# Kernel optimization log

Measured on AMD Instinct MI355X. Metric: run time of the kernel, lower is better.

The kernel has to match this reference:

```python
import jax, jax.numpy as jnp
import numpy as np

D, HEADS, PTS, NQ, BEV_H, BEV_W, NCLS, BS, NL = 256, 8, 4, 900, 200, 200, 10, 4, 6
HD = D // HEADS
PC = (-51.2, -51.2, -5.0, 51.2, 51.2, 3.0)


def _ln(x, w, b):
    m = x.mean(-1, keepdims=True)
    v = ((x - m) ** 2).mean(-1, keepdims=True)
    return (x - m) * jax.lax.rsqrt(v + 1e-5) * w + b


def _inv_sig(x, eps=1e-5):
    x = jnp.clip(x, 0.0, 1.0)
    return jnp.log(jnp.clip(x, eps, None) / jnp.clip(1.0 - x, eps, None))


def _mha(q_in, k_in, v_in, in_w, in_b, out_w, out_b):
    # torch nn.MultiheadAttention (eval, dropout=0): packed in_proj (3D,D)
    b, n, _ = q_in.shape
    qw, kw, vw = jnp.split(in_w, 3, axis=0)
    qb, kb, vb = jnp.split(in_b, 3, axis=0)
    q = (q_in @ qw.T + qb).reshape(b, n, HEADS, HD)
    k = (k_in @ kw.T + kb).reshape(b, k_in.shape[1], HEADS, HD)
    v = (v_in @ vw.T + vb).reshape(b, v_in.shape[1], HEADS, HD)
    s = jnp.einsum('bqhd,bkhd->bhqk', q, k) * (1.0 / float(np.sqrt(HD)))
    a = jax.nn.softmax(s, axis=-1)
    o = jnp.einsum('bhqk,bkhd->bqhd', a, v).reshape(b, n, D)
    return o @ out_w.T + out_b


def _deform_attn(q, identity, value, ref2d, off_w, off_b, aw_w, aw_b, vp_w, vp_b, op_w, op_b):
    # CustomMSDeformableAttention, num_levels=1, num_points=4; bilinear grid_sample
    # semantics: align_corners=False, zero padding.
    b, n, _ = q.shape
    hw = value.shape[1]
    v = (value @ vp_w.T + vp_b).reshape(b, hw, HEADS, HD)
    vg = v.transpose(0, 2, 1, 3)  # (b, heads, HW, hd)
    off = (q @ off_w.T + off_b).reshape(b, n, HEADS, PTS, 2)
    aw = jax.nn.softmax((q @ aw_w.T + aw_b).reshape(b, n, HEADS, PTS), axis=-1)
    norm = jnp.array([BEV_W, BEV_H], jnp.float32)  # offset_normalizer = (W, H)
    loc = ref2d[:, :, None, None, :] + off / norm  # (b,n,heads,P,2) in [0,1]
    # grid_sample align_corners=False pixel coords
    x = (loc[..., 0] * BEV_W - 0.5).transpose(0, 2, 1, 3)  # (b,heads,n,P)
    y = (loc[..., 1] * BEV_H - 0.5).transpose(0, 2, 1, 3)
    x0 = jnp.floor(x); y0 = jnp.floor(y)
    x0i = x0.astype(jnp.int32); y0i = y0.astype(jnp.int32)
    fx = x - x0; fy = y - y0
    sampled = jnp.zeros(x.shape + (HD,), q.dtype)
    for dy, wy in ((0, 1.0 - fy), (1, fy)):
        for dx, wx in ((0, 1.0 - fx), (1, fx)):
            xi = x0i + dx; yi = y0i + dy
            valid = (xi >= 0) & (xi < BEV_W) & (yi >= 0) & (yi < BEV_H)
            lin = jnp.clip(yi, 0, BEV_H - 1) * BEV_W + jnp.clip(xi, 0, BEV_W - 1)
            g = jnp.take_along_axis(vg, lin.reshape(b, HEADS, n * PTS)[..., None], axis=2)
            g = g.reshape(b, HEADS, n, PTS, HD)
            sampled = sampled + g * (wx * wy * valid)[..., None]
    out = jnp.einsum('bhnpc,bnhp->bnhc', sampled, aw).reshape(b, n, D)
    return identity + (out @ op_w.T + op_b)


def _forward(bev_embed, query_embed, ref_w, ref_b, sa_in_w, sa_in_b, sa_out_w, sa_out_b,
             ln_w, ln_b, off_w, off_b, aw_w, aw_b, vproj_w, vproj_b, oproj_w, oproj_b,
             ffn_w1, ffn_b1, ffn_w2, ffn_b2, reg_w1, reg_b1, reg_w2, reg_b2, reg_w3, reg_b3,
             cls_w1, cls_b1, cls_w2, cls_b2, cls_w3, cls_b3, cls_ln_w, cls_ln_b):
    bs = bev_embed.shape[0]
    qpos = jnp.broadcast_to(query_embed[None, :, :D], (bs, NQ, D))
    q = jnp.broadcast_to(query_embed[None, :, D:], (bs, NQ, D))
    ref = jax.nn.sigmoid(qpos @ ref_w.T + ref_b)  # (bs, NQ, 3)
    init_ref = ref

    def reg_apply(i, x):
        h = jax.nn.relu(x @ reg_w1[i].T + reg_b1[i])
        h = jax.nn.relu(h @ reg_w2[i].T + reg_b2[i])
        return h @ reg_w3[i].T + reg_b3[i]

    hs, refs = [], []
    for i in range(NL):
        # self_attn -> norm
        sa = _mha(q + qpos, q + qpos, q, sa_in_w[i], sa_in_b[i], sa_out_w[i], sa_out_b[i])
        q = _ln(q + sa, ln_w[i, 0], ln_b[i, 0])
        # cross_attn (deformable) -> norm; query_pos added inside attn, identity pre-pos
        ca = _deform_attn(q + qpos, q, bev_embed, ref[..., :2], off_w[i], off_b[i],
                          aw_w[i], aw_b[i], vproj_w[i], vproj_b[i], oproj_w[i], oproj_b[i])
        q = _ln(ca, ln_w[i, 1], ln_b[i, 1])
        # ffn -> norm
        ff = jax.nn.relu(q @ ffn_w1[i].T + ffn_b1[i]) @ ffn_w2[i].T + ffn_b2[i]
        q = _ln(q + ff, ln_w[i, 2], ln_b[i, 2])
        # iterative box refinement (detached in torch)
        tmp = reg_apply(i, q)
        new_ref = jnp.concatenate([
            jax.nn.sigmoid(tmp[..., :2] + _inv_sig(ref[..., :2])),
            jax.nn.sigmoid(tmp[..., 4:5] + _inv_sig(ref[..., 2:3]))], axis=-1)
        ref = jax.lax.stop_gradient(new_ref)
        hs.append(q)
        refs.append(ref)

    cls_list, coord_list = [], []
    for i in range(NL):
        r = _inv_sig(init_ref if i == 0 else refs[i - 1])
        x = hs[i]
        h = jax.nn.relu(_ln(x @ cls_w1[i].T + cls_b1[i], cls_ln_w[i, 0], cls_ln_b[i, 0]))
        h = jax.nn.relu(_ln(h @ cls_w2[i].T + cls_b2[i], cls_ln_w[i, 1], cls_ln_b[i, 1]))
        cls = h @ cls_w3[i].T + cls_b3[i]
        tmp = reg_apply(i, x)
        xy = jax.nn.sigmoid(tmp[..., 0:2] + r[..., 0:2])
        z = jax.nn.sigmoid(tmp[..., 4:5] + r[..., 2:3])
        cx = xy[..., 0:1] * (PC[3] - PC[0]) + PC[0]
        cy = xy[..., 1:2] * (PC[4] - PC[1]) + PC[1]
        cz = z * (PC[5] - PC[2]) + PC[2]
        coord = jnp.concatenate([cx, cy, tmp[..., 2:4], cz, tmp[..., 5:]], axis=-1)
        cls_list.append(cls)
        coord_list.append(coord)
    # (NL, bs, NQ, NCLS+10): classes and boxes concatenated on last dim
    return jnp.concatenate([jnp.stack(cls_list), jnp.stack(coord_list)], axis=-1)


def setup_inputs() -> dict:
    key = jax.random.key(0)
    ks = iter(jax.random.split(key, 64))
    def nrm(shape, s=0.02):
        return jax.random.normal(next(ks), shape, jnp.float32) * s
    d, C = D, NCLS
    return dict(
        bev_embed=jax.random.normal(next(ks), (BS, BEV_H * BEV_W, d), jnp.float32),
        query_embed=nrm((NQ, 2 * d), 1.0),
        ref_w=nrm((3, d)), ref_b=jnp.zeros((3,), jnp.float32),
        sa_in_w=nrm((NL, 3 * d, d)), sa_in_b=jnp.zeros((NL, 3 * d), jnp.float32),
        sa_out_w=nrm((NL, d, d)), sa_out_b=jnp.zeros((NL, d), jnp.float32),
        ln_w=jnp.ones((NL, 3, d), jnp.float32), ln_b=jnp.zeros((NL, 3, d), jnp.float32),
        off_w=nrm((NL, HEADS * PTS * 2, d)), off_b=nrm((NL, HEADS * PTS * 2), 0.5),
        aw_w=nrm((NL, HEADS * PTS, d)), aw_b=jnp.zeros((NL, HEADS * PTS), jnp.float32),
        vproj_w=nrm((NL, d, d)), vproj_b=jnp.zeros((NL, d), jnp.float32),
        oproj_w=nrm((NL, d, d)), oproj_b=jnp.zeros((NL, d), jnp.float32),
        ffn_w1=nrm((NL, 2 * d, d)), ffn_b1=jnp.zeros((NL, 2 * d), jnp.float32),
        ffn_w2=nrm((NL, d, 2 * d)), ffn_b2=jnp.zeros((NL, d), jnp.float32),
        reg_w1=nrm((NL, d, d)), reg_b1=jnp.zeros((NL, d), jnp.float32),
        reg_w2=nrm((NL, d, d)), reg_b2=jnp.zeros((NL, d), jnp.float32),
        reg_w3=nrm((NL, 10, d)), reg_b3=jnp.zeros((NL, 10), jnp.float32),
        cls_w1=nrm((NL, d, d)), cls_b1=jnp.zeros((NL, d), jnp.float32),
        cls_w2=nrm((NL, d, d)), cls_b2=jnp.zeros((NL, d), jnp.float32),
        cls_w3=nrm((NL, C, d)), cls_b3=jnp.zeros((NL, C), jnp.float32),
        cls_ln_w=jnp.ones((NL, 2, d), jnp.float32), cls_ln_b=jnp.zeros((NL, 2, d), jnp.float32),
    )


def reference(bev_embed, query_embed, ref_w, ref_b, sa_in_w, sa_in_b, sa_out_w, sa_out_b,
              ln_w, ln_b, off_w, off_b, aw_w, aw_b, vproj_w, vproj_b, oproj_w, oproj_b,
              ffn_w1, ffn_b1, ffn_w2, ffn_b2, reg_w1, reg_b1, reg_w2, reg_b2, reg_w3, reg_b3,
              cls_w1, cls_b1, cls_w2, cls_b2, cls_w3, cls_b3, cls_ln_w, cls_ln_b):
    return _forward(bev_embed, query_embed, ref_w, ref_b, sa_in_w, sa_in_b, sa_out_w, sa_out_b,
                    ln_w, ln_b, off_w, off_b, aw_w, aw_b, vproj_w, vproj_b, oproj_w, oproj_b,
                    ffn_w1, ffn_b1, ffn_w2, ffn_b2, reg_w1, reg_b1, reg_w2, reg_b2, reg_w3, reg_b3,
                    cls_w1, cls_b1, cls_w2, cls_b2, cls_w3, cls_b3, cls_ln_w, cls_ln_b)
```

## Files before the change

### kernel.cpp

```cpp
#include <hip/hip_runtime.h>
#include <math.h>

#define DD 256
#define NQQ 900
#define NBS 4
#define NLAYER 6
#define BEVH 200
#define BEVW 200
#define ROWS (NBS*NQQ)
#define BIGN (1<<30)

typedef __attribute__((ext_vector_type(8))) short bf16x8;
typedef __attribute__((ext_vector_type(4))) float f32x4;

__device__ __forceinline__ float sigmoidf_(float x){ return 1.0f/(1.0f+expf(-x)); }
__device__ __forceinline__ float invsigf_(float x){
  x = fminf(fmaxf(x,0.0f),1.0f);
  float lo = fmaxf(x,1e-5f), hi = fmaxf(1.0f-x,1e-5f);
  return logf(lo/hi);
}
__device__ __forceinline__ unsigned f2bf1(float x){
  unsigned u = __float_as_uint(x);
  return (u + 0x7fffu + ((u>>16)&1u)) >> 16;
}
__device__ __forceinline__ unsigned pk2(float a, float b){
  return f2bf1(a) | (f2bf1(b)<<16);
}
__device__ __forceinline__ float bf2f(unsigned u){ return __uint_as_float(u<<16); }
__device__ __forceinline__ ushort4 pk4(float4 y){
  ushort4 o; o.x=(ushort)f2bf1(y.x); o.y=(ushort)f2bf1(y.y);
  o.z=(ushort)f2bf1(y.z); o.w=(ushort)f2bf1(y.w); return o;
}

__global__ __launch_bounds__(256) void gemm_k(
    const float* __restrict__ A, int lda,
    const float* __restrict__ W, const float* __restrict__ B,
    float* __restrict__ Y, int M, int N, int K, int ldy, int act)
{
  __shared__ float As[2][32][66];
  __shared__ float Ws[2][32][66];
  const int t = threadIdx.x;
  const int m0 = blockIdx.x*64, n0 = blockIdx.y*64;
  const int lr = t >> 2, kq = (t & 3) << 3;
  const int tx = t & 15, ty = t >> 4;
  const bool aok = (m0 + lr) < M;
  const bool wok = (n0 + lr) < N;
  const float* ap  = A + (size_t)(m0+lr)*lda + kq;
  const float* wp  = W + (size_t)(n0+lr)*K + kq;
  float4 pa[2], pw[2];
  auto loadch = [&](int kc) {
    #pragma unroll
    for (int i=0;i<2;++i) {
      pa[i] = aok ? *(const float4*)(ap + kc + i*4) : make_float4(0,0,0,0);
      pw[i] = wok ? *(const float4*)(wp + kc + i*4) : make_float4(0,0,0,0);
    }
  };
  auto storech = [&](int bf) {
    #pragma unroll
    for (int i=0;i<2;++i) {
      const int kk = kq + i*4;
      As[bf][kk+0][lr]=pa[i].x; As[bf][kk+1][lr]=pa[i].y;
      As[bf][kk+2][lr]=pa[i].z; As[bf][kk+3][lr]=pa[i].w;
      Ws[bf][kk+0][lr]=pw[i].x; Ws[bf][kk+1][lr]=pw[i].y;
      Ws[bf][kk+2][lr]=pw[i].z; Ws[bf][kk+3][lr]=pw[i].w;
    }
  };
  float acc[4][4] = {};
  loadch(0); storech(0); __syncthreads();
  const int NC = K >> 5;
  for (int c=0; c<NC; ++c) {
    if (c+1 < NC) loadch((c+1) << 5);
    const int bf = c & 1;
    #pragma unroll
    for (int k=0;k<32;++k) {
      const float4 a4 = *(const float4*)&As[bf][k][ty<<2];
      const float4 w4 = *(const float4*)&Ws[bf][k][tx<<2];
      const float av[4] = {a4.x,a4.y,a4.z,a4.w};
      const float wv[4] = {w4.x,w4.y,w4.z,w4.w};
      #pragma unroll
      for (int r=0;r<4;++r)
        #pragma unroll
        for (int cc=0;cc<4;++cc) acc[r][cc] += av[r]*wv[cc];
    }
    if (c+1 < NC) { storech((c+1)&1); __syncthreads(); }
  }
  const int gn0 = n0 + (tx<<2);
  #pragma unroll
  for (int r=0;r<4;++r) {
    const int gm = m0 + (ty<<2) + r;
    if (gm >= M) continue;
    for (int cc=0; cc<4 && gn0+cc<N; ++cc) {
      float x = acc[r][cc] + (B ? B[gn0+cc] : 0.0f);
      if (act==1) x = fmaxf(x,0.0f);
      else if (act==2) x = sigmoidf_(x);
      Y[(size_t)gm*ldy + gn0+cc] = x;
    }
  }
}

template<int BM>
__global__ __launch_bounds__(256) void gemmb_k(
    const ushort* __restrict__ A0, const ushort* __restrict__ A1, int NA, int lda,
    const ushort* __restrict__ W0, const ushort* __restrict__ W1, int NW,
    const float* __restrict__ B0, const float* __restrict__ B1, int NB,
    void* __restrict__ Y0, int ldy0, int obf0,
    void* __restrict__ Y1, int ldy1, int obf1, int NY,
    int M, int N, int K, int reluN)
{
  __shared__ ushort As[2][BM*32];
  __shared__ ushort Bs[2][2048];
  const int t = threadIdx.x;
  const int m0 = blockIdx.x*BM, n0 = blockIdx.y*64;
  const ushort* A = (n0 < NA) ? A0 : A1;
  const int srow = t>>2, scb = t&3;
  const int wrow = n0 + srow;
  const bool wok = wrow < N;
  const ushort* wp = (wrow < NW) ? (W0 + (size_t)wrow*K + scb*8)
                                 : (W1 + (size_t)(wrow-NW)*K + scb*8);
  bool aok; const ushort* ap;
  if constexpr (BM==64) { aok = (m0+srow)<M; }
  else { aok = (t<128) && (m0+srow)<M; }
  ap = A + (size_t)(m0 + (aok?srow:0))*lda + scb*8;
  const int sidx = srow*32 + ((scb ^ (srow&3))<<3);
  const bf16x8 zf = {0,0,0,0,0,0,0,0};

  bf16x8 pa, pw;
  auto loadg = [&](int kc){
    pa = aok ? *(const bf16x8*)(ap+kc) : zf;
    pw = wok ? *(const bf16x8*)(wp+kc) : zf;
  };
  auto writes = [&](int bf){
    if (BM==64 || t<128) *(bf16x8*)&As[bf][sidx] = pa;
    *(bf16x8*)&Bs[bf][sidx] = pw;
  };

  const int wv = t>>6, lane = t&63;
  const int fm = lane&15, kb = lane>>4;

  auto writeout = [&](float x, int row, int col){
    if (row >= M || col >= N) return;
    if (col < reluN) x = fmaxf(x, 0.0f);
    if (col < NY) {
      if (obf0) ((ushort*)Y0)[(size_t)row*ldy0 + col] = (ushort)f2bf1(x);
      else      ((float*)Y0)[(size_t)row*ldy0 + col] = x;
    } else {
      const int c2 = col - NY;
      if (obf1) ((ushort*)Y1)[(size_t)row*ldy1 + c2] = (ushort)f2bf1(x);
      else      ((float*)Y1)[(size_t)row*ldy1 + c2] = x;
    }
  };

  const int NS = K>>5;
  if constexpr (BM==64) {
    const int wr = wv>>1, wc = wv&1;
    const int arow0 = wr*32 + fm, arow1 = arow0 + 16;
    const int bcol0 = wc*32 + fm, bcol1 = bcol0 + 16;
    const int ai0 = arow0*32 + ((kb^(arow0&3))<<3);
    const int ai1 = arow1*32 + ((kb^(arow1&3))<<3);
    const int bi0 = bcol0*32 + ((kb^(bcol0&3))<<3);
    const int bi1 = bcol1*32 + ((kb^(bcol1&3))<<3);
    f32x4 acc00={0,0,0,0}, acc01={0,0,0,0}, acc10={0,0,0,0}, acc11={0,0,0,0};
    loadg(0); writes(0); __syncthreads();
    for (int s=0; s<NS; ++s) {
      if (s+1<NS) loadg((s+1)<<5);
      const int bf = s&1;
      bf16x8 a0 = *(bf16x8*)&As[bf][ai0];
      bf16x8 a1 = *(bf16x8*)&As[bf][ai1];
      bf16x8 b0 = *(bf16x8*)&Bs[bf][bi0];
      bf16x8 b1 = *(bf16x8*)&Bs[bf][bi1];
      acc00 = __builtin_amdgcn_mfma_f32_16x16x32_bf16(a0,b0,acc00,0,0,0);
      acc01 = __builtin_amdgcn_mfma_f32_16x16x32_bf16(a0,b1,acc01,0,0,0);
      acc10 = __builtin_amdgcn_mfma_f32_16x16x32_bf16(a1,b0,acc10,0,0,0);
      acc11 = __builtin_amdgcn_mfma_f32_16x16x32_bf16(a1,b1,acc11,0,0,0);
      if (s+1<NS) { __syncthreads(); writes((s+1)&1); __syncthreads(); }
    }
    #pragma unroll
    for (int fr=0; fr<2; ++fr)
      #pragma unroll
      for (int fc=0; fc<2; ++fc) {
        const f32x4 av = fr ? (fc ? acc11 : acc10) : (fc ? acc01 : acc00);
        const int col = n0 + wc*32 + fc*16 + fm;
        const float bias = (col<N) ? ((col<NB) ? B0[col] : B1[col-NB]) : 0.0f;
        #pragma unroll
        for (int r=0; r<4; ++r)
          writeout(av[r] + bias, m0 + wr*32 + fr*16 + kb*4 + r, col);
      }
  } else {
    const int ai0 = fm*32 + ((kb^(fm&3))<<3);
    const int ai1 = (fm+16)*32 + ((kb^(fm&3))<<3);
    const int bcol = wv*16 + fm;
    const int bi = bcol*32 + ((kb^(bcol&3))<<3);
    f32x4 acc0={0,0,0,0}, acc1={0,0,0,0};
    loadg(0); writes(0); __syncthreads();
    for (int s=0; s<NS; ++s) {
      if (s+1<NS) loadg((s+1)<<5);
      const int bf = s&1;
      bf16x8 a0 = *(bf16x8*)&As[bf][ai0];
      bf16x8 a1 = *(bf16x8*)&As[bf][ai1];
      bf16x8 b  = *(bf16x8*)&Bs[bf][bi];
      acc0 = __builtin_amdgcn_mfma_f32_16x16x32_bf16(a0,b,acc0,0,0,0);
      acc1 = __builtin_amdgcn_mfma_f32_16x16x32_bf16(a1,b,acc1,0,0,0);
      if (s+1<NS) { __syncthreads(); writes((s+1)&1); __syncthreads(); }
    }
    const int col = n0 + wv*16 + fm;
    const float bias = (col<N) ? ((col<NB) ? B0[col] : B1[col-NB]) : 0.0f;
    #pragma unroll
    for (int r=0; r<4; ++r) {
      writeout(acc0[r] + bias, m0 + kb*4 + r, col);
      writeout(acc1[r] + bias, m0 + 16 + kb*4 + r, col);
    }
  }
}

__global__ __launch_bounds__(256) void attn3_k(
    const ushort* __restrict__ QKb, const ushort* __restrict__ Vb, ushort* __restrict__ Ob)
{
  const int b = blockIdx.x >> 3, h = blockIdx.x & 7;
  const int wv = threadIdx.x >> 6, lane = threadIdx.x & 63;
  const int qt = blockIdx.y*64 + wv*16;
  if (qt >= NQQ) return;
  const int lq = lane & 15, lg = lane >> 4;
  const int q = qt + lq;

  bf16x8 qf = *(const bf16x8*)(QKb + (size_t)(b*NQQ + min(q, NQQ-1))*512 + h*32 + lg*8);
  f32x4 ot0 = {0.f,0.f,0.f,0.f}, ot1 = {0.f,0.f,0.f,0.f};
  float m = -3e38f, l = 0.0f;

  const ushort* kb = QKb + (size_t)b*NQQ*512 + 256 + h*32 + lg*8;
  const ushort* vb = Vb  + (size_t)b*NQQ*256 + h*32;
  const int pbase = (lq + ((lg&1)<<5)) << 2;
  const bool hiC = (lg >> 1);

  for (int k0 = 0; k0 < NQQ; k0 += 32) {
    const int r0 = min(k0 + lq, NQQ-1), r1 = min(k0 + 16 + lq, NQQ-1);
    bf16x8 kf0 = *(const bf16x8*)(kb + (size_t)r0*512);
    bf16x8 kf1 = *(const bf16x8*)(kb + (size_t)r1*512);
    const f32x4 z = {0.f,0.f,0.f,0.f};
    f32x4 s0 = __builtin_amdgcn_mfma_f32_16x16x32_bf16(kf0, qf, z, 0, 0, 0);
    f32x4 s1 = __builtin_amdgcn_mfma_f32_16x16x32_bf16(kf1, qf, z, 0, 0, 0);
    const float sc = 0.17677669529663687f;
    float p0[4], p1[4];
    #pragma unroll
    for (int r=0;r<4;++r) { p0[r] = s0[r]*sc; p1[r] = s1[r]*sc; }
    if (k0 + 32 > NQQ) {
      #pragma unroll
      for (int r=0;r<4;++r) {
        if (k0 + 4*lg + r      >= NQQ) p0[r] = -3e38f;
        if (k0 + 16 + 4*lg + r >= NQQ) p1[r] = -3e38f;
      }
    }
    float cm = fmaxf(fmaxf(fmaxf(p0[0],p0[1]),fmaxf(p0[2],p0[3])),
                     fmaxf(fmaxf(p1[0],p1[1]),fmaxf(p1[2],p1[3])));
    cm = fmaxf(cm, __shfl_xor(cm, 16));
    cm = fmaxf(cm, __shfl_xor(cm, 32));
    const float mn = fmaxf(m, cm);
    const float corr = __expf(m - mn);
    m = mn;
    float rs = 0.0f;
    #pragma unroll
    for (int r=0;r<4;++r) { p0[r] = __expf(p0[r]-mn); rs += p0[r]; }
    #pragma unroll
    for (int r=0;r<4;++r) { p1[r] = __expf(p1[r]-mn); rs += p1[r]; }
    rs += __shfl_xor(rs, 16);
    rs += __shfl_xor(rs, 32);
    l = l*corr + rs;
    ot0 *= corr; ot1 *= corr;

    const int c00 = (int)pk2(p0[0],p0[1]), c01 = (int)pk2(p0[2],p0[3]);
    const int c10 = (int)pk2(p1[0],p1[1]), c11 = (int)pk2(p1[2],p1[3]);
    const int A0 = __builtin_amdgcn_ds_bpermute(pbase,    c00);
    const int B0 = __builtin_amdgcn_ds_bpermute(pbase,    c10);
    const int A1 = __builtin_amdgcn_ds_bpermute(pbase,    c01);
    const int B1 = __builtin_amdgcn_ds_bpermute(pbase,    c11);
    const int A2 = __builtin_amdgcn_ds_bpermute(pbase+64, c00);
    const int B2 = __builtin_amdgcn_ds_bpermute(pbase+64, c10);
    const int A3 = __builtin_amdgcn_ds_bpermute(pbase+64, c01);
    const int B3 = __builtin_amdgcn_ds_bpermute(pbase+64, c11);
    union { bf16x8 v; int u[4]; } pv;
    pv.u[0] = hiC ? B0 : A0; pv.u[1] = hiC ? B1 : A1;
    pv.u[2] = hiC ? B2 : A2; pv.u[3] = hiC ? B3 : A3;

    bf16x8 vf0, vf1;
    {
      union { bf16x8 v; unsigned u[4]; } u0, u1;
      const int kvb = k0 + 8*lg;
      #pragma unroll
      for (int jj=0;jj<4;++jj) {
        const int ra = min(kvb + 2*jj,   NQQ-1);
        const int rb = min(kvb + 2*jj+1, NQQ-1);
        u0.u[jj] = (unsigned)vb[(size_t)ra*256 + lq]      | ((unsigned)vb[(size_t)rb*256 + lq]<<16);
        u1.u[jj] = (unsigned)vb[(size_t)ra*256 + 16 + lq] | ((unsigned)vb[(size_t)rb*256 + 16 + lq]<<16);
      }
      vf0 = u0.v; vf1 = u1.v;
    }
    ot0 = __builtin_amdgcn_mfma_f32_16x16x32_bf16(vf0, pv.v, ot0, 0, 0, 0);
    ot1 = __builtin_amdgcn_mfma_f32_16x16x32_bf16(vf1, pv.v, ot1, 0, 0, 0);
  }
  if (q < NQQ) {
    const float inv = 1.0f / l;
    ushort* op = Ob + (size_t)(b*NQQ + q)*256 + h*32;
    uint2 w0, w1;
    w0.x = pk2(ot0[0]*inv, ot0[1]*inv); w0.y = pk2(ot0[2]*inv, ot0[3]*inv);
    w1.x = pk2(ot1[0]*inv, ot1[1]*inv); w1.y = pk2(ot1[2]*inv, ot1[3]*inv);
    *(uint2*)(op + 4*lg)      = w0;
    *(uint2*)(op + 16 + 4*lg) = w1;
  }
}

__global__ __launch_bounds__(256) void ln_k(
    const float* X, int xld, const float* R,
    const float* __restrict__ w, const float* __restrict__ b,
    float* Y, ushort* Yb, const float* qpos, ushort* Ypb, int relu)
{
  const int row = blockIdx.x*4 + (threadIdx.x>>6);
  const int lane = threadIdx.x & 63;
  if (row >= ROWS) return;
  float4 x = *(const float4*)(X + (size_t)row*xld + (lane<<2));
  if (R) { const float4 r = *(const float4*)(R + (size_t)row*256 + (lane<<2)); x.x+=r.x; x.y+=r.y; x.z+=r.z; x.w+=r.w; }
  float s = x.x+x.y+x.z+x.w;
  #pragma unroll
  for (int o=32;o>0;o>>=1) s += __shfl_xor(s,o);
  const float mean = s * (1.0f/256.0f);
  float4 d; d.x=x.x-mean; d.y=x.y-mean; d.z=x.z-mean; d.w=x.w-mean;
  float s2 = d.x*d.x+d.y*d.y+d.z*d.z+d.w*d.w;
  #pragma unroll
  for (int o=32;o>0;o>>=1) s2 += __shfl_xor(s2,o);
  const float rs = rsqrtf(s2*(1.0f/256.0f) + 1e-5f);
  const float4 wv = *(const float4*)(w + (lane<<2));
  const float4 bv = *(const float4*)(b + (lane<<2));
  float4 y;
  y.x = d.x*rs*wv.x + bv.x; y.y = d.y*rs*wv.y + bv.y;
  y.z = d.z*rs*wv.z + bv.z; y.w = d.w*rs*wv.w + bv.w;
  if (relu) { y.x=fmaxf(y.x,0.f); y.y=fmaxf(y.y,0.f); y.z=fmaxf(y.z,0.f); y.w=fmaxf(y.w,0.f); }
  if (Y)  *(float4*)(Y + (size_t)row*256 + (lane<<2)) = y;
  if (Yb) *(ushort4*)(Yb + (size_t)row*256 + (lane<<2)) = pk4(y);
  if (Ypb) {
    const float4 qp = *(const float4*)(qpos + (size_t)row*256 + (lane<<2));
    float4 z; z.x=y.x+qp.x; z.y=y.y+qp.y; z.z=y.z+qp.z; z.w=y.w+qp.w;
    *(ushort4*)(Ypb + (size_t)row*256 + (lane<<2)) = pk4(z);
  }
}

__global__ __launch_bounds__(512) void gather_k(
    const ushort* __restrict__ bevb, const float* __restrict__ offaw,
    const float* __restrict__ ref, ushort* __restrict__ rr, float* __restrict__ sumw)
{
  const int row = blockIdx.x;
  const int h = threadIdx.x >> 6, lane = threadIdx.x & 63;
  const int b = row / NQQ;
  const float refx = ref[row*3+0], refy = ref[row*3+1];
  const float* oa = offaw + (size_t)row*96;
  float aw[4];
  {
    const float a0=oa[64+h*4+0], a1=oa[64+h*4+1], a2=oa[64+h*4+2], a3=oa[64+h*4+3];
    const float mx = fmaxf(fmaxf(a0,a1), fmaxf(a2,a3));
    const float e0=__expf(a0-mx), e1=__expf(a1-mx), e2=__expf(a2-mx), e3=__expf(a3-mx);
    const float inv = 1.0f/(e0+e1+e2+e3);
    aw[0]=e0*inv; aw[1]=e1*inv; aw[2]=e2*inv; aw[3]=e3*inv;
  }
  float r0=0.f, r1=0.f, r2=0.f, r3=0.f, sacc=0.f;
  const ushort* bb = bevb + (size_t)b*BEVH*BEVW*DD;
  #pragma unroll
  for (int p=0;p<4;++p) {
    const float ox = oa[h*8+p*2+0], oy = oa[h*8+p*2+1];
    const float x = (refx + ox*(1.0f/BEVW))*BEVW - 0.5f;
    const float y = (refy + oy*(1.0f/BEVH))*BEVH - 0.5f;
    const float x0f = floorf(x), y0f = floorf(y);
    const int x0 = (int)x0f, y0 = (int)y0f;
    const float fx = x - x0f, fy = y - y0f;
    #pragma unroll
    for (int dy=0;dy<2;++dy) {
      #pragma unroll
      for (int dx=0;dx<2;++dx) {
        const int xi = x0+dx, yi = y0+dy;
        if (xi < 0 || xi >= BEVW || yi < 0 || yi >= BEVH) continue;
        const float wgt = (dx ? fx : 1.0f-fx) * (dy ? fy : 1.0f-fy) * aw[p];
        const ushort4 g = *(const ushort4*)(bb + (size_t)(yi*BEVW + xi)*DD + (lane<<2));
        r0 += wgt*bf2f(g.x); r1 += wgt*bf2f(g.y);
        r2 += wgt*bf2f(g.z); r3 += wgt*bf2f(g.w);
        sacc += wgt;
      }
    }
  }
  ushort4 o;
  o.x = (ushort)f2bf1(r0); o.y = (ushort)f2bf1(r1);
  o.z = (ushort)f2bf1(r2); o.w = (ushort)f2bf1(r3);
  *(ushort4*)&rr[((size_t)h*ROWS + row)*256 + (lane<<2)] = o;
  if (lane == 0) sumw[h*ROWS + row] = sacc;
}

__global__ __launch_bounds__(256) void proj_k(
    const ushort* __restrict__ rr, const float* __restrict__ sumw,
    const float* __restrict__ vpw, const float* __restrict__ vpb,
    ushort* __restrict__ sampb)
{
  const int h = blockIdx.y;
  __shared__ float Ws[32*257];
  for (int i=threadIdx.x; i<8192; i+=256) {
    const int c = i>>8, k = i&255;
    Ws[c*257+k] = vpw[(size_t)((h<<5)+c)*256 + k];
  }
  __syncthreads();
  const int wv = threadIdx.x>>6, lane = threadIdx.x&63;
  const int c = lane&31, half = lane>>5;
  const float bias = vpb[(h<<5)+c];
  #pragma unroll
  for (int j=0;j<8;++j) {
    const int r = blockIdx.x*32 + wv*8 + j;
    if (r >= ROWS) break;
    const ushort* rp = rr + ((size_t)h*ROWS + r)*256 + half*128;
    const float* wb = &Ws[c*257 + half*128];
    float acc = 0.0f;
    #pragma unroll
    for (int jj=0;jj<32;++jj) {
      const uint2 u = *(const uint2*)(rp + jj*4);
      acc += bf2f(u.x & 0xffffu) * wb[jj*4+0];
      acc += bf2f(u.x >> 16)     * wb[jj*4+1];
      acc += bf2f(u.y & 0xffffu) * wb[jj*4+2];
      acc += bf2f(u.y >> 16)     * wb[jj*4+3];
    }
    acc += __shfl_xor(acc, 32);
    if (half == 0) sampb[(size_t)r*256 + (h<<5) + c] = (ushort)f2bf1(acc + bias*sumw[h*ROWS + r]);
  }
}

__global__ __launch_bounds__(256) void regcls3_k(
    const float* __restrict__ rc2,
    const float* __restrict__ lnw, const float* __restrict__ lnb,
    const float* __restrict__ rw3, const float* __restrict__ rb3,
    const float* __restrict__ cw3, const float* __restrict__ cb3,
    float* __restrict__ ref, float* __restrict__ outL)
{
  __shared__ float Wr[10*272];
  __shared__ float Wc[10*272];
  for (int i=threadIdx.x; i<2560; i+=256) {
    const int o = i>>8, k = i&255;
    const int si = o*272 + (k>>6)*68 + (k&63);
    Wr[si] = rw3[i]; Wc[si] = cw3[i];
  }
  __syncthreads();
  const int t = threadIdx.x;
  const int row = t>>3, g = (t>>2)&1, sl = t&3;
  const int R = blockIdx.x*32 + row;
  const bool act = R < ROWS;
  const float* base = rc2 + (size_t)(act?R:0)*512 + g*256 + sl*64;
  float4 v[16];
  #pragma unroll
  for (int jj=0;jj<16;++jj) v[jj] = *(const float4*)(base + 4*jj);
  float s1 = 0.f, s2 = 0.f;
  #pragma unroll
  for (int jj=0;jj<16;++jj) {
    s1 += v[jj].x+v[jj].y+v[jj].z+v[jj].w;
    s2 += v[jj].x*v[jj].x+v[jj].y*v[jj].y+v[jj].z*v[jj].z+v[jj].w*v[jj].w;
  }
  s1 += __shfl_xor(s1,1); s1 += __shfl_xor(s1,2);
  s2 += __shfl_xor(s2,1); s2 += __shfl_xor(s2,2);
  if (g) {
    const float mean = s1*(1.0f/256.0f);
    const float var = s2*(1.0f/256.0f) - mean*mean;
    const float rs = rsqrtf(var + 1e-5f);
    #pragma unroll
    for (int jj=0;jj<16;++jj) {
      const float4 w4 = *(const float4*)(lnw + sl*64 + 4*jj);
      const float4 b4 = *(const float4*)(lnb + sl*64 + 4*jj);
      v[jj].x = fmaxf((v[jj].x-mean)*rs*w4.x + b4.x, 0.f);
      v[jj].y = fmaxf((v[jj].y-mean)*rs*w4.y + b4.y, 0.f);
      v[jj].z = fmaxf((v[jj].z-mean)*rs*w4.z + b4.z, 0.f);
      v[jj].w = fmaxf((v[jj].w-mean)*rs*w4.w + b4.w, 0.f);
    }
  }
  const float* Wg = g ? Wc : Wr;
  float acc[10] = {};
  #pragma unroll
  for (int jj=0;jj<16;++jj) {
    #pragma unroll
    for (int o=0;o<10;++o) {
      const float4 w = *(const float4*)&Wg[o*272 + sl*68 + 4*jj];
      acc[o] += v[jj].x*w.x + v[jj].y*w.y + v[jj].z*w.z + v[jj].w*w.w;
    }
  }
  #pragma unroll
  for (int o=0;o<10;++o) {
    acc[o] += __shfl_xor(acc[o], 1);
    acc[o] += __shfl_xor(acc[o], 2);
  }
  if (act && sl == 0) {
    if (g) {
      float* oc = outL + (size_t)R*20;
      #pragma unroll
      for (int o=0;o<10;++o) oc[o] = acc[o] + cb3[o];
    } else {
      float tt[10];
      #pragma unroll
      for (int o=0;o<10;++o) tt[o] = acc[o] + rb3[o];
      const float rx = invsigf_(ref[R*3+0]);
      const float ry = invsigf_(ref[R*3+1]);
      const float rz = invsigf_(ref[R*3+2]);
      const float nx = sigmoidf_(tt[0]+rx);
      const float ny = sigmoidf_(tt[1]+ry);
      const float nz = sigmoidf_(tt[4]+rz);
      ref[R*3+0]=nx; ref[R*3+1]=ny; ref[R*3+2]=nz;
      float* o = outL + (size_t)R*20 + 10;
      o[0]=nx*102.4f-51.2f; o[1]=ny*102.4f-51.2f; o[2]=tt[2]; o[3]=tt[3];
      o[4]=nz*8.0f-5.0f; o[5]=tt[5]; o[6]=tt[6]; o[7]=tt[7]; o[8]=tt[8]; o[9]=tt[9];
    }
  }
}

__global__ void init_k(const float* __restrict__ qe, float* __restrict__ qpos,
                       float* __restrict__ q, ushort* __restrict__ qb, ushort* __restrict__ qpb)
{
  const int t = blockIdx.x*blockDim.x + threadIdx.x;
  const int row = t >> 6; const int cc = (t & 63) << 2;
  const int n = row % NQQ;
  const float4 vp = *(const float4*)(qe + (size_t)n*512 + cc);
  const float4 vq = *(const float4*)(qe + (size_t)n*512 + 256 + cc);
  *(float4*)(qpos + (size_t)row*256 + cc) = vp;
  *(float4*)(q    + (size_t)row*256 + cc) = vq;
  *(ushort4*)(qb  + (size_t)row*256 + cc) = pk4(vq);
  float4 s; s.x=vq.x+vp.x; s.y=vq.y+vp.y; s.z=vq.z+vp.z; s.w=vq.w+vp.w;
  *(ushort4*)(qpb + (size_t)row*256 + cc) = pk4(s);
}

__global__ void prep_k(const float* __restrict__ ow, const float* __restrict__ ob,
                       const float* __restrict__ aw, const float* __restrict__ ab,
                       const float* __restrict__ rw, const float* __restrict__ rb,
                       const float* __restrict__ cw, const float* __restrict__ cb,
                       ushort* cwAb, float* cbA, ushort* cwBb, float* cbB)
{
  const int i = blockIdx.x*blockDim.x + threadIdx.x;
  if (i < 6*96*256) {
    const int l = i/(96*256), r = (i/256)%96, k = i%256;
    const float v = (r<64) ? ow[((size_t)l*64 + r)*256 + k] : aw[((size_t)l*32 + (r-64))*256 + k];
    cwAb[i] = (ushort)f2bf1(v);
  }
  if (i < 576) { const int l = i/96, r = i%96; cbA[i] = (r<64) ? ob[l*64+r] : ab[l*32 + r-64]; }
  if (i < 6*512*256) {
    const int l = i/(512*256), r = (i/256)%512, k = i%256;
    const float v = (r<256) ? rw[((size_t)l*256+r)*256+k] : cw[((size_t)l*256 + (r-256))*256 + k];
    cwBb[i] = (ushort)f2bf1(v);
  }
  if (i < 3072) { const int l = i/512, r = i%512; cbB[i] = (r<256) ? rb[l*256+r] : cb[l*256 + r-256]; }
}

__global__ void cvtw_k(const float* __restrict__ s1, const float* __restrict__ s2,
                       const float* __restrict__ s3, const float* __restrict__ s4,
                       const float* __restrict__ s5, const float* __restrict__ s6,
                       const float* __restrict__ s7, ushort* __restrict__ dst)
{
  const int i4 = (blockIdx.x*256 + threadIdx.x)*4;
  if (i4 >= 4325376) return;
  const float* src; int lo;
  if      (i4 < 1179648) { src=s1; lo=i4; }
  else if (i4 < 1572864) { src=s2; lo=i4-1179648; }
  else if (i4 < 1966080) { src=s3; lo=i4-1572864; }
  else if (i4 < 2752512) { src=s4; lo=i4-1966080; }
  else if (i4 < 3538944) { src=s5; lo=i4-2752512; }
  else if (i4 < 3932160) { src=s6; lo=i4-3538944; }
  else                   { src=s7; lo=i4-3932160; }
  const float4 v = *(const float4*)(src+lo);
  *(ushort4*)(dst+i4) = pk4(v);
}

__global__ void cvtbev_k(const float* __restrict__ bev, ushort* __restrict__ bevb)
{
  const size_t i = ((size_t)blockIdx.x*256 + threadIdx.x)*8;
  const float4 a = *(const float4*)(bev+i);
  const float4 b = *(const float4*)(bev+i+4);
  *(ushort4*)(bevb+i)   = pk4(a);
  *(ushort4*)(bevb+i+4) = pk4(b);
}

extern "C" void kernel_launch(void* const* d_in, const int* in_sizes, int n_in,
                              void* d_out, int out_size, void* d_ws, size_t ws_size,
                              hipStream_t stream)
{
  const float* bev      = (const float*)d_in[0];
  const float* qe       = (const float*)d_in[1];
  const float* ref_w    = (const float*)d_in[2];
  const float* ref_b    = (const float*)d_in[3];
  const float* sa_in_w  = (const float*)d_in[4];
  const float* sa_in_b  = (const float*)d_in[5];
  const float* sa_out_w = (const float*)d_in[6];
  const float* sa_out_b = (const float*)d_in[7];
  const float* ln_w     = (const float*)d_in[8];
  const float* ln_b     = (const float*)d_in[9];
  const float* off_w    = (const float*)d_in[10];
  const float* off_b    = (const float*)d_in[11];
  const float* aw_w     = (const float*)d_in[12];
  const float* aw_b     = (const float*)d_in[13];
  const float* vproj_w  = (const float*)d_in[14];
  const float* vproj_b  = (const float*)d_in[15];
  const float* oproj_w  = (const float*)d_in[16];
  const float* oproj_b  = (const float*)d_in[17];
  const float* ffn_w1   = (const float*)d_in[18];
  const float* ffn_b1   = (const float*)d_in[19];
  const float* ffn_w2   = (const float*)d_in[20];
  const float* ffn_b2   = (const float*)d_in[21];
  const float* reg_w1   = (const float*)d_in[22];
  const float* reg_b1   = (const float*)d_in[23];
  const float* reg_w2   = (const float*)d_in[24];
  const float* reg_b2   = (const float*)d_in[25];
  const float* reg_w3   = (const float*)d_in[26];
  const float* reg_b3   = (const float*)d_in[27];
  const float* cls_w1   = (const float*)d_in[28];
  const float* cls_b1   = (const float*)d_in[29];
  const float* cls_w2   = (const float*)d_in[30];
  const float* cls_b2   = (const float*)d_in[31];
  const float* cls_w3   = (const float*)d_in[32];
  const float* cls_b3   = (const float*)d_in[33];
  const float* cls_ln_w = (const float*)d_in[34];
  const float* cls_ln_b = (const float*)d_in[35];
  float* out = (float*)d_out;

  float* ws    = (float*)d_ws;
  float* qpos  = ws;
  float* q     = qpos + 921600;
  float* tA    = q    + 921600;
  float* tB    = tA   + 921600;
  float* rc2   = tB   + 921600;
  float* cls1f = rc2  + 1843200;
  float* offaw = cls1f+ 921600;
  float* ref   = offaw+ 345600;
  float* sumw  = ref  + 10800;
  float* cbA   = sumw + 28800;
  float* cbB   = cbA  + 576;
  ushort* usb  = (ushort*)(ws + 6840048);
  ushort* QKb  = usb;
  ushort* Vb   = usb + 1843200;
  ushort* tAb  = usb + 2764800;
  ushort* W5b  = usb + 3686400;
  ushort* sampb= usb + 5529600;
  ushort* qb   = usb + 6451200;
  ushort* qpb  = usb + 7372800;
  ushort* clsb = usb + 8294400;
  ushort* regb = usb + 9216000;
  ushort* rr   = usb + 10137600;
  ushort* bevb = usb + 17510400;
  ushort* wbf  = usb + 58470400;
  ushort* siwb = wbf;
  ushort* sowb = wbf + 1179648;
  ushort* opwb = wbf + 1572864;
  ushort* f1wb = wbf + 1966080;
  ushort* f2wb = wbf + 2752512;
  ushort* r2wb = wbf + 3538944;
  ushort* c2wb = wbf + 3932160;
  ushort* cwAb = wbf + 4325376;
  ushort* cwBb = wbf + 4472832;

  auto G = [&](int BM, const ushort* A0, const ushort* A1, int NA, int lda,
               const ushort* W0, const ushort* W1, int NW,
               const float* B0, const float* B1, int NB,
               void* Y0, int ldy0, int obf0,
               void* Y1, int ldy1, int obf1, int NY,
               int M, int N, int K, int reluN) {
    dim3 grid((M+BM-1)/BM, (N+63)/64);
    if (BM==64)
      gemmb_k<64><<<grid, 256, 0, stream>>>(A0,A1,NA,lda,W0,W1,NW,B0,B1,NB,
                                            Y0,ldy0,obf0,Y1,ldy1,obf1,NY,M,N,K,reluN);
    else
      gemmb_k<32><<<grid, 256, 0, stream>>>(A0,A1,NA,lda,W0,W1,NW,B0,B1,NB,
                                            Y0,ldy0,obf0,Y1,ldy1,obf1,NY,M,N,K,reluN);
  };

  cvtbev_k<<<20000, 256, 0, stream>>>(bev, bevb);
  cvtw_k<<<4224, 256, 0, stream>>>(sa_in_w, sa_out_w, oproj_w, ffn_w1, ffn_w2, reg_w2, cls_w2, wbf);
  prep_k<<<3072, 256, 0, stream>>>(off_w, off_b, aw_w, aw_b, reg_w1, reg_b1, cls_w1, cls_b1,
                                   cwAb, cbA, cwBb, cbB);
  init_k<<<900, 256, 0, stream>>>(qe, qpos, q, qb, qpb);
  {
    dim3 grid((ROWS+63)/64, 1);
    gemm_k<<<grid, 256, 0, stream>>>(qpos, 256, ref_w, ref_b, ref, ROWS, 3, 256, 3, 2);
  }

  for (int i=0;i<NLAYER;++i) {
    const float* sib = sa_in_b + (size_t)i*768;
    const ushort* siw = siwb + (size_t)i*196608;
    G(64, qpb, qb, 512, 256, siw, siw, BIGN, sib, sib, BIGN,
      QKb, 512, 1, Vb, 256, 1, 512, ROWS, 768, 256, 0);
    attn3_k<<<dim3(32,15), 256, 0, stream>>>(QKb, Vb, tAb);
    G(32, tAb, tAb, BIGN, 256, sowb + (size_t)i*65536, nullptr, BIGN,
      sa_out_b + (size_t)i*256, nullptr, BIGN,
      tB, 256, 0, nullptr, 0, 0, BIGN, ROWS, 256, 256, 0);
    ln_k<<<900, 256, 0, stream>>>(tB, 256, q, ln_w + (size_t)(i*3+0)*256, ln_b + (size_t)(i*3+0)*256,
                                  q, nullptr, qpos, qpb, 0);
    G(32, qpb, qpb, BIGN, 256, cwAb + (size_t)i*24576, nullptr, BIGN,
      cbA + i*96, nullptr, BIGN,
      offaw, 96, 0, nullptr, 0, 0, BIGN, ROWS, 96, 256, 0);
    gather_k<<<ROWS, 512, 0, stream>>>(bevb, offaw, ref, rr, sumw);
    proj_k<<<dim3(113,8), 256, 0, stream>>>(rr, sumw,
        vproj_w + (size_t)i*65536, vproj_b + (size_t)i*256, sampb);
    G(32, sampb, sampb, BIGN, 256, opwb + (size_t)i*65536, nullptr, BIGN,
      oproj_b + (size_t)i*256, nullptr, BIGN,
      tA, 256, 0, nullptr, 0, 0, BIGN, ROWS, 256, 256, 0);
    ln_k<<<900, 256, 0, stream>>>(tA, 256, q, ln_w + (size_t)(i*3+1)*256, ln_b + (size_t)(i*3+1)*256,
                                  q, qb, nullptr, nullptr, 0);
    G(64, qb, qb, BIGN, 256, f1wb + (size_t)i*131072, nullptr, BIGN,
      ffn_b1 + (size_t)i*512, nullptr, BIGN,
      W5b, 512, 1, nullptr, 0, 0, BIGN, ROWS, 512, 256, 512);
    G(32, W5b, W5b, BIGN, 512, f2wb + (size_t)i*131072, nullptr, BIGN,
      ffn_b2 + (size_t)i*256, nullptr, BIGN,
      tA, 256, 0, nullptr, 0, 0, BIGN, ROWS, 256, 512, 0);
    ln_k<<<900, 256, 0, stream>>>(tA, 256, q, ln_w + (size_t)(i*3+2)*256, ln_b + (size_t)(i*3+2)*256,
                                  q, qb, qpos, qpb, 0);
    G(64, qb, qb, BIGN, 256, cwBb + (size_t)i*131072, nullptr, BIGN,
      cbB + i*512, nullptr, BIGN,
      regb, 256, 1, cls1f, 256, 0, 256, ROWS, 512, 256, 256);
    ln_k<<<900, 256, 0, stream>>>(cls1f, 256, nullptr,
                                  cls_ln_w + (size_t)(i*2+0)*256, cls_ln_b + (size_t)(i*2+0)*256,
                                  nullptr, clsb, nullptr, nullptr, 1);
    G(64, regb, clsb, 256, 256,
      r2wb + (size_t)i*65536, c2wb + (size_t)i*65536, 256,
      reg_b2 + (size_t)i*256, cls_b2 + (size_t)i*256, 256,
      rc2, 512, 0, nullptr, 0, 0, BIGN, ROWS, 512, 256, 256);
    regcls3_k<<<(ROWS+31)/32, 256, 0, stream>>>(rc2,
        cls_ln_w + (size_t)(i*2+1)*256, cls_ln_b + (size_t)(i*2+1)*256,
        reg_w3 + (size_t)i*2560, reg_b3 + (size_t)i*10,
        cls_w3 + (size_t)i*2560, cls_b3 + (size_t)i*10,
        ref, out + (size_t)i*ROWS*20);
  }
}
```

Measured before the change: 1.380 ms.

## Fold value projection into output projection and stage attention K/V in LDS

The per-head value projection and the output projection are algebraically merged into a single precomputed weight of width 2080 (8 heads × 256 plus bias columns). The separate proj_k pass and the sampb intermediate are removed, and the output GEMM now runs directly on the gathered features with K=2080. This drops one kernel and the fp32 FMA loop but makes the output GEMM about eight times larger in K and rounds the combined weights to bf16. In addition, the self-attention kernel now double-buffers K and transposed V tiles in shared memory instead of making strided scalar global loads of V.

```diff
diff --git a/kernel.cpp b/kernel.cpp
--- a/kernel.cpp
+++ b/kernel.cpp
@@ -9,6 +9,7 @@
 #define BEVW 200
 #define ROWS (NBS*NQQ)
 #define BIGN (1<<30)
+#define KDEF 2080
 
 typedef __attribute__((ext_vector_type(8))) short bf16x8;
 typedef __attribute__((ext_vector_type(4))) float f32x4;
@@ -217,24 +218,47 @@
 {
   const int b = blockIdx.x >> 3, h = blockIdx.x & 7;
   const int wv = threadIdx.x >> 6, lane = threadIdx.x & 63;
+  const int t = threadIdx.x;
   const int qt = blockIdx.y*64 + wv*16;
-  if (qt >= NQQ) return;
   const int lq = lane & 15, lg = lane >> 4;
   const int q = qt + lq;
+
+  __shared__ ushort Ks[2][32*40];
+  __shared__ ushort Vt[2][32*34];
 
   bf16x8 qf = *(const bf16x8*)(QKb + (size_t)(b*NQQ + min(q, NQQ-1))*512 + h*32 + lg*8);
   f32x4 ot0 = {0.f,0.f,0.f,0.f}, ot1 = {0.f,0.f,0.f,0.f};
   float m = -3e38f, l = 0.0f;
 
-  const ushort* kb = QKb + (size_t)b*NQQ*512 + 256 + h*32 + lg*8;
-  const ushort* vb = Vb  + (size_t)b*NQQ*256 + h*32;
+  const ushort* kg = QKb + (size_t)b*NQQ*512 + 256 + h*32;
+  const ushort* vg = Vb  + (size_t)b*NQQ*256 + h*32;
+  const int srow = t>>3, sc4 = (t&7)*4;
+
+  ushort4 kv, vv;
+  auto sload = [&](int k0){
+    const int gr = min(k0 + srow, NQQ-1);
+    kv = *(const ushort4*)(kg + (size_t)gr*512 + sc4);
+    vv = *(const ushort4*)(vg + (size_t)gr*256 + sc4);
+  };
+  auto swrite = [&](int bf){
+    *(ushort4*)&Ks[bf][srow*40 + sc4] = kv;
+    Vt[bf][(sc4+0)*34 + srow] = vv.x;
+    Vt[bf][(sc4+1)*34 + srow] = vv.y;
+    Vt[bf][(sc4+2)*34 + srow] = vv.z;
+    Vt[bf][(sc4+3)*34 + srow] = vv.w;
+  };
+
   const int pbase = (lq + ((lg&1)<<5)) << 2;
   const bool hiC = (lg >> 1);
-
-  for (int k0 = 0; k0 < NQQ; k0 += 32) {
-    const int r0 = min(k0 + lq, NQQ-1), r1 = min(k0 + 16 + lq, NQQ-1);
-    bf16x8 kf0 = *(const bf16x8*)(kb + (size_t)r0*512);
-    bf16x8 kf1 = *(const bf16x8*)(kb + (size_t)r1*512);
+  const int NC = (NQQ + 31) >> 5;
+
+  sload(0); swrite(0); __syncthreads();
+  for (int c = 0; c < NC; ++c) {
+    const int k0 = c<<5;
+    if (c+1 < NC) sload((c+1)<<5);
+    const int bf = c&1;
+    bf16x8 kf0 = *(bf16x8*)&Ks[bf][lq*40 + lg*8];
+    bf16x8 kf1 = *(bf16x8*)&Ks[bf][(16+lq)*40 + lg*8];
     const f32x4 z = {0.f,0.f,0.f,0.f};
     f32x4 s0 = __builtin_amdgcn_mfma_f32_16x16x32_bf16(kf0, qf, z, 0, 0, 0);
     f32x4 s1 = __builtin_amdgcn_mfma_f32_16x16x32_bf16(kf1, qf, z, 0, 0, 0);
@@ -283,20 +307,19 @@
     bf16x8 vf0, vf1;
     {
       union { bf16x8 v; unsigned u[4]; } u0, u1;
-      const int kvb = k0 + 8*lg;
+      const int rb = 8*lg;
       #pragma unroll
       for (int jj=0;jj<4;++jj) {
-        const int ra = min(kvb + 2*jj,   NQQ-1);
-        const int rb = min(kvb + 2*jj+1, NQQ-1);
-        u0.u[jj] = (unsigned)vb[(size_t)ra*256 + lq]      | ((unsigned)vb[(size_t)rb*256 + lq]<<16);
-        u1.u[jj] = (unsigned)vb[(size_t)ra*256 + 16 + lq] | ((unsigned)vb[(size_t)rb*256 + 16 + lq]<<16);
+        u0.u[jj] = *(const unsigned*)&Vt[bf][lq*34 + rb + 2*jj];
+        u1.u[jj] = *(const unsigned*)&Vt[bf][(16+lq)*34 + rb + 2*jj];
       }
       vf0 = u0.v; vf1 = u1.v;
     }
     ot0 = __builtin_amdgcn_mfma_f32_16x16x32_bf16(vf0, pv.v, ot0, 0, 0, 0);
     ot1 = __builtin_amdgcn_mfma_f32_16x16x32_bf16(vf1, pv.v, ot1, 0, 0, 0);
-  }
-  if (q < NQQ) {
+    if (c+1 < NC) { __syncthreads(); swrite((c+1)&1); __syncthreads(); }
+  }
+  if (q < NQQ && qt < NQQ) {
     const float inv = 1.0f / l;
     ushort* op = Ob + (size_t)(b*NQQ + q)*256 + h*32;
     uint2 w0, w1;
@@ -336,14 +359,14 @@
   if (Yb) *(ushort4*)(Yb + (size_t)row*256 + (lane<<2)) = pk4(y);
   if (Ypb) {
     const float4 qp = *(const float4*)(qpos + (size_t)row*256 + (lane<<2));
-    float4 z; z.x=y.x+qp.x; z.y=y.y+qp.y; z.z=y.z+qp.z; z.w=y.w+qp.w;
-    *(ushort4*)(Ypb + (size_t)row*256 + (lane<<2)) = pk4(z);
+    float4 zz; zz.x=y.x+qp.x; zz.y=y.y+qp.y; zz.z=y.z+qp.z; zz.w=y.w+qp.w;
+    *(ushort4*)(Ypb + (size_t)row*256 + (lane<<2)) = pk4(zz);
   }
 }
 
 __global__ __launch_bounds__(512) void gather_k(
     const ushort* __restrict__ bevb, const float* __restrict__ offaw,
-    const float* __restrict__ ref, ushort* __restrict__ rr, float* __restrict__ sumw)
+    const float* __restrict__ ref, ushort* __restrict__ rr)
 {
   const int row = blockIdx.x;
   const int h = threadIdx.x >> 6, lane = threadIdx.x & 63;
@@ -385,43 +408,61 @@
   ushort4 o;
   o.x = (ushort)f2bf1(r0); o.y = (ushort)f2bf1(r1);
   o.z = (ushort)f2bf1(r2); o.w = (ushort)f2bf1(r3);
-  *(ushort4*)&rr[((size_t)h*ROWS + row)*256 + (lane<<2)] = o;
-  if (lane == 0) sumw[h*ROWS + row] = sacc;
-}
-
-__global__ __launch_bounds__(256) void proj_k(
-    const ushort* __restrict__ rr, const float* __restrict__ sumw,
-    const float* __restrict__ vpw, const float* __restrict__ vpb,
-    ushort* __restrict__ sampb)
-{
-  const int h = blockIdx.y;
-  __shared__ float Ws[32*257];
-  for (int i=threadIdx.x; i<8192; i+=256) {
-    const int c = i>>8, k = i&255;
-    Ws[c*257+k] = vpw[(size_t)((h<<5)+c)*256 + k];
+  ushort* rrow = rr + (size_t)row*KDEF;
+  *(ushort4*)&rrow[h*256 + (lane<<2)] = o;
+  if (lane == 0) rrow[2048 + h] = (ushort)f2bf1(sacc);
+  else if (lane < 4) rrow[2048 + lane*8 + h] = 0;
+}
+
+__global__ __launch_bounds__(256) void wcomb_k(
+    const float* __restrict__ opw, const float* __restrict__ vpw,
+    ushort* __restrict__ Wfull)
+{
+  const int l = blockIdx.z, h = blockIdx.y;
+  const int ct = blockIdx.x & 3, kt = blockIdx.x >> 2;
+  __shared__ float Ao[64][33];
+  __shared__ float Bo[32][65];
+  const int t = threadIdx.x;
+  for (int i=t; i<2048; i+=256) {
+    const int r = i>>5, j = i&31;
+    Ao[r][j] = opw[(size_t)l*65536 + (size_t)(ct*64 + r)*256 + h*32 + j];
+  }
+  for (int i=t; i<2048; i+=256) {
+    const int j = i>>6, kk = i&63;
+    Bo[j][kk] = vpw[(size_t)l*65536 + (size_t)(h*32 + j)*256 + kt*64 + kk];
   }
   __syncthreads();
-  const int wv = threadIdx.x>>6, lane = threadIdx.x&63;
-  const int c = lane&31, half = lane>>5;
-  const float bias = vpb[(h<<5)+c];
-  #pragma unroll
-  for (int j=0;j<8;++j) {
-    const int r = blockIdx.x*32 + wv*8 + j;
-    if (r >= ROWS) break;
-    const ushort* rp = rr + ((size_t)h*ROWS + r)*256 + half*128;
-    const float* wb = &Ws[c*257 + half*128];
-    float acc = 0.0f;
-    #pragma unroll
-    for (int jj=0;jj<32;++jj) {
-      const uint2 u = *(const uint2*)(rp + jj*4);
-      acc += bf2f(u.x & 0xffffu) * wb[jj*4+0];
-      acc += bf2f(u.x >> 16)     * wb[jj*4+1];
-      acc += bf2f(u.y & 0xffffu) * wb[jj*4+2];
-      acc += bf2f(u.y >> 16)     * wb[jj*4+3];
-    }
-    acc += __shfl_xor(acc, 32);
-    if (half == 0) sampb[(size_t)r*256 + (h<<5) + c] = (ushort)f2bf1(acc + bias*sumw[h*ROWS + r]);
-  }
+  const int tx = t&15, ty = t>>4;
+  float acc[4][4] = {};
+  for (int j=0;j<32;++j) {
+    float a[4], bv[4];
+    #pragma unroll
+    for (int r=0;r<4;++r) a[r] = Ao[ty*4+r][j];
+    #pragma unroll
+    for (int cc=0;cc<4;++cc) bv[cc] = Bo[j][tx*4+cc];
+    #pragma unroll
+    for (int r=0;r<4;++r)
+      #pragma unroll
+      for (int cc=0;cc<4;++cc) acc[r][cc] += a[r]*bv[cc];
+  }
+  #pragma unroll
+  for (int r=0;r<4;++r)
+    #pragma unroll
+    for (int cc=0;cc<4;++cc)
+      Wfull[((size_t)l*256 + ct*64+ty*4+r)*KDEF + h*256 + kt*64 + tx*4+cc] = (ushort)f2bf1(acc[r][cc]);
+}
+
+__global__ void wcombB_k(const float* __restrict__ opw, const float* __restrict__ vpb,
+                         ushort* __restrict__ Wfull)
+{
+  const int l = blockIdx.x; const int c = threadIdx.x;
+  ushort* wr = Wfull + ((size_t)l*256 + c)*KDEF;
+  for (int h=0; h<8; ++h) {
+    float s = 0.f;
+    for (int j=0;j<32;++j) s += opw[(size_t)l*65536 + (size_t)c*256 + h*32+j] * vpb[l*256 + h*32+j];
+    wr[2048 + h] = (ushort)f2bf1(s);
+  }
+  for (int zz=2056; zz<KDEF; ++zz) wr[zz] = 0;
 }
 
 __global__ __launch_bounds__(256) void regcls3_k(
@@ -622,31 +663,29 @@
   float* cls1f = rc2  + 1843200;
   float* offaw = cls1f+ 921600;
   float* ref   = offaw+ 345600;
-  float* sumw  = ref  + 10800;
-  float* cbA   = sumw + 28800;
+  float* cbA   = ref  + 10800;
   float* cbB   = cbA  + 576;
-  ushort* usb  = (ushort*)(ws + 6840048);
+  ushort* usb  = (ushort*)(ws + 6811248);
+  ushort* rr   = usb;
   ushort* QKb  = usb;
   ushort* Vb   = usb + 1843200;
   ushort* tAb  = usb + 2764800;
   ushort* W5b  = usb + 3686400;
-  ushort* sampb= usb + 5529600;
-  ushort* qb   = usb + 6451200;
-  ushort* qpb  = usb + 7372800;
-  ushort* clsb = usb + 8294400;
-  ushort* regb = usb + 9216000;
-  ushort* rr   = usb + 10137600;
-  ushort* bevb = usb + 17510400;
-  ushort* wbf  = usb + 58470400;
+  ushort* clsb = usb + 5529600;
+  ushort* regb = usb + 6451200;
+  ushort* qb   = usb + 7488000;
+  ushort* qpb  = usb + 8409600;
+  ushort* bevb = usb + 9331200;
+  ushort* wbf  = usb + 50291200;
   ushort* siwb = wbf;
   ushort* sowb = wbf + 1179648;
-  ushort* opwb = wbf + 1572864;
   ushort* f1wb = wbf + 1966080;
   ushort* f2wb = wbf + 2752512;
   ushort* r2wb = wbf + 3538944;
   ushort* c2wb = wbf + 3932160;
   ushort* cwAb = wbf + 4325376;
   ushort* cwBb = wbf + 4472832;
+  ushort* Wfull= wbf + 5259264;
 
   auto G = [&](int BM, const ushort* A0, const ushort* A1, int NA, int lda,
                const ushort* W0, const ushort* W1, int NW,
@@ -667,6 +706,8 @@
   cvtw_k<<<4224, 256, 0, stream>>>(sa_in_w, sa_out_w, oproj_w, ffn_w1, ffn_w2, reg_w2, cls_w2, wbf);
   prep_k<<<3072, 256, 0, stream>>>(off_w, off_b, aw_w, aw_b, reg_w1, reg_b1, cls_w1, cls_b1,
                                    cwAb, cbA, cwBb, cbB);
+  wcomb_k<<<dim3(16,8,6), 256, 0, stream>>>(oproj_w, vproj_w, Wfull);
+  wcombB_k<<<6, 256, 0, stream>>>(oproj_w, vproj_b, Wfull);
   init_k<<<900, 256, 0, stream>>>(qe, qpos, q, qb, qpb);
   {
     dim3 grid((ROWS+63)/64, 1);
@@ -687,12 +728,10 @@
     G(32, qpb, qpb, BIGN, 256, cwAb + (size_t)i*24576, nullptr, BIGN,
       cbA + i*96, nullptr, BIGN,
       offaw, 96, 0, nullptr, 0, 0, BIGN, ROWS, 96, 256, 0);
-    gather_k<<<ROWS, 512, 0, stream>>>(bevb, offaw, ref, rr, sumw);
-    proj_k<<<dim3(113,8), 256, 0, stream>>>(rr, sumw,
-        vproj_w + (size_t)i*65536, vproj_b + (size_t)i*256, sampb);
-    G(32, sampb, sampb, BIGN, 256, opwb + (size_t)i*65536, nullptr, BIGN,
+    gather_k<<<ROWS, 512, 0, stream>>>(bevb, offaw, ref, rr);
+    G(32, rr, rr, BIGN, KDEF, Wfull + (size_t)i*256*KDEF, nullptr, BIGN,
       oproj_b + (size_t)i*256, nullptr, BIGN,
-      tA, 256, 0, nullptr, 0, 0, BIGN, ROWS, 256, 256, 0);
+      tA, 256, 0, nullptr, 0, 0, BIGN, ROWS, 256, KDEF, 0);
     ln_k<<<900, 256, 0, stream>>>(tA, 256, q, ln_w + (size_t)(i*3+1)*256, ln_b + (size_t)(i*3+1)*256,
                                   q, qb, nullptr, nullptr, 0);
     G(64, qb, qb, BIGN, 256, f1wb + (size_t)i*131072, nullptr, BIGN,
```

Result: faster. 1.169 ms (median of 2 runs) (-15.3%).
